# Optimization experiments

Measured on AMD Instinct MI355X. Metric: run time of the kernel, lower is better.

## Reference

```python
import jax, jax.numpy as jnp
import numpy as np

B, T, C, H = 2, 2048, 768, 12
HD = C // H  # head dim = 64
EPS = 1e-5


def layer_norm(x, g, b):
    mu = jnp.mean(x, axis=-1, keepdims=True)
    var = jnp.var(x, axis=-1, keepdims=True)
    return (x - mu) * jax.lax.rsqrt(var + EPS) * g + b


def setup_inputs() -> dict:
    key = jax.random.key(0)
    ks = jax.random.split(key, 5)
    s = 0.02
    return {
        "x": jax.random.normal(ks[0], (B, T, C), jnp.float32),
        "ln1_g": jnp.ones((C,), jnp.float32),
        "ln1_b": jnp.zeros((C,), jnp.float32),
        "W_qkv": jax.random.normal(ks[1], (C, 3 * C), jnp.float32) * s,
        "W_attn_proj": jax.random.normal(ks[2], (C, C), jnp.float32) * s,
        "ln2_g": jnp.ones((C,), jnp.float32),
        "ln2_b": jnp.zeros((C,), jnp.float32),
        "W_fc": jax.random.normal(ks[3], (C, 4 * C), jnp.float32) * s,
        "W_mlp_proj": jax.random.normal(ks[4], (4 * C, C), jnp.float32) * s,
    }


def attention(x, W_qkv, W_attn_proj):
    b, t, c = x.shape
    qkv = x @ W_qkv  # [B,T,3C]
    q, k, v = jnp.split(qkv, 3, axis=-1)
    # [B,H,T,HD]
    q = q.reshape(b, t, H, HD).transpose(0, 2, 1, 3)
    k = k.reshape(b, t, H, HD).transpose(0, 2, 1, 3)
    v = v.reshape(b, t, H, HD).transpose(0, 2, 1, 3)
    att = jnp.einsum("bhqd,bhkd->bhqk", q, k) * (1.0 / np.sqrt(HD).astype(np.float32))
    causal = jnp.tril(jnp.ones((t, t), jnp.bool_))
    att = jnp.where(causal, att, jnp.finfo(att.dtype).min)
    att = jax.nn.softmax(att, axis=-1)
    y = jnp.einsum("bhqk,bhkd->bhqd", att, v)
    y = y.transpose(0, 2, 1, 3).reshape(b, t, c)
    return y @ W_attn_proj


def mlp(x, W_fc, W_mlp_proj):
    h = jax.nn.gelu(x @ W_fc, approximate=False)
    return h @ W_mlp_proj


def reference(x, ln1_g, ln1_b, W_qkv, W_attn_proj, ln2_g, ln2_b, W_fc, W_mlp_proj):
    x = x + attention(layer_norm(x, ln1_g, ln1_b), W_qkv, W_attn_proj)
    x = x + mlp(layer_norm(x, ln2_g, ln2_b), W_fc, W_mlp_proj)
    return x
```

## Files before the change

kernel.cpp:

```cpp
#include <hip/hip_runtime.h>
#include <cstdint>
#include <cstddef>

typedef unsigned short u16;
typedef __attribute__((ext_vector_type(4))) float f32x4;
typedef __attribute__((ext_vector_type(8))) short bf16x8;

__device__ __forceinline__ u16 f2bf(float f) {
  unsigned int u = __builtin_bit_cast(unsigned int, f);
  u += 0x7fffu + ((u >> 16) & 1u);
  return (u16)(u >> 16);
}

__device__ __forceinline__ void gl_lds16(const u16* g, u16* lds_base) {
  __builtin_amdgcn_global_load_lds(
      (const __attribute__((address_space(1))) unsigned int*)g,
      (__attribute__((address_space(3))) unsigned int*)lds_base, 16, 0, 0);
}

__global__ __launch_bounds__(256) void transpose_w(const float* __restrict__ src,
                                                   u16* __restrict__ dst,
                                                   int K, int N) {
  __shared__ float tile[32][33];
  int n0 = blockIdx.x * 32, k0 = blockIdx.y * 32;
  int tx = threadIdx.x & 31, ty = threadIdx.x >> 5;
#pragma unroll
  for (int i = 0; i < 4; ++i)
    tile[ty + i * 8][tx] = src[(size_t)(k0 + ty + i * 8) * N + n0 + tx];
  __syncthreads();
#pragma unroll
  for (int i = 0; i < 4; ++i)
    dst[(size_t)(n0 + ty + i * 8) * K + k0 + tx] = f2bf(tile[tx][ty + i * 8]);
}

__global__ __launch_bounds__(256) void transpose_v(const u16* __restrict__ qkvb,
                                                   u16* __restrict__ vt) {
  __shared__ u16 tile[64 * 72];
  int t0 = blockIdx.x * 64;
  int bh = blockIdx.y;
  int b = bh / 12, h = bh % 12;
  int tid = threadIdx.x;
  int c8 = tid & 7, r = tid >> 3;
#pragma unroll
  for (int i = 0; i < 2; ++i) {
    int rr = r + i * 32;
    *(uint4*)&tile[rr * 72 + c8 * 8] =
        *(const uint4*)&qkvb[(size_t)(b * 2048 + t0 + rr) * 2304 + 1536 + h * 64 + c8 * 8];
  }
  __syncthreads();
#pragma unroll
  for (int i = 0; i < 2; ++i) {
    int dr = r + i * 32;
    u16 tmp[8];
#pragma unroll
    for (int j = 0; j < 8; ++j) tmp[j] = tile[(c8 * 8 + j) * 72 + dr];
    *(uint4*)&vt[((size_t)bh * 64 + dr) * 2048 + t0 + c8 * 8] = *(uint4*)tmp;
  }
}

__global__ void zero_counter(unsigned int* c) {
  if (threadIdx.x == 0) *c = 0u;
}

__global__ __launch_bounds__(192) void ln_rows(const float* __restrict__ x,
                                               const float* __restrict__ g,
                                               const float* __restrict__ bb,
                                               u16* __restrict__ out) {
  int row = blockIdx.x;
  int t = threadIdx.x;
  float4 v = *(const float4*)(x + (size_t)row * 768 + t * 4);
  float s = v.x + v.y + v.z + v.w;
  float sq = v.x * v.x + v.y * v.y + v.z * v.z + v.w * v.w;
#pragma unroll
  for (int o = 32; o > 0; o >>= 1) {
    s += __shfl_down(s, o);
    sq += __shfl_down(sq, o);
  }
  __shared__ float ss[3], s2[3];
  int w = t >> 6;
  if ((t & 63) == 0) { ss[w] = s; s2[w] = sq; }
  __syncthreads();
  s = ss[0] + ss[1] + ss[2];
  sq = s2[0] + s2[1] + s2[2];
  float mu = s * (1.f / 768.f);
  float var = sq * (1.f / 768.f) - mu * mu;
  float rs = rsqrtf(var + 1e-5f);
  float4 gv = *(const float4*)(g + t * 4);
  float4 bv = *(const float4*)(bb + t * 4);
  u16 o4[4];
  o4[0] = f2bf((v.x - mu) * rs * gv.x + bv.x);
  o4[1] = f2bf((v.y - mu) * rs * gv.y + bv.y);
  o4[2] = f2bf((v.z - mu) * rs * gv.z + bv.z);
  o4[3] = f2bf((v.w - mu) * rs * gv.w + bv.w);
  *(uint2*)(out + (size_t)row * 768 + t * 4) = *(uint2*)o4;
}

template <int EPI, int TN>
__global__ __launch_bounds__(256, 3) void gemm_bt(const u16* __restrict__ A,
                                                  const u16* __restrict__ BT,
                                                  int M, int N, int K,
                                                  float* __restrict__ outF,
                                                  u16* __restrict__ outB,
                                                  const float* __restrict__ res) {
  constexpr int MT = (TN == 128) ? 4 : 2;
  __shared__ __align__(16) u16 Al[128 * 64];
  __shared__ __align__(16) u16 Bl[TN * 64];
  int tid = threadIdx.x;
  int lane = tid & 63, w = tid >> 6;
  int l16 = lane & 15, quad = lane >> 4;
  int swz = l16 & 7;
  int wm = (TN == 128) ? (w >> 1) : w;
  int wn = (TN == 128) ? (w & 1) : 0;
  size_t rowA0 = (size_t)blockIdx.y * 128;
  size_t rowB0 = (size_t)blockIdx.x * TN;

  f32x4 acc[MT][4] = {};

  for (int k0 = 0; k0 < K; k0 += 64) {
    __syncthreads();
#pragma unroll
    for (int i = 0; i < 4; ++i) {
      int cbase = (i * 4 + w) * 64;
      int chunk = cbase + lane;
      int r = chunk >> 3, c8 = (chunk & 7) ^ (r & 7);
      gl_lds16(&A[(rowA0 + r) * (size_t)K + k0 + c8 * 8], &Al[cbase * 8]);
    }
#pragma unroll
    for (int i = 0; i < TN / 32; ++i) {
      int cbase = (i * 4 + w) * 64;
      int chunk = cbase + lane;
      int r = chunk >> 3, c8 = (chunk & 7) ^ (r & 7);
      gl_lds16(&BT[(rowB0 + r) * (size_t)K + k0 + c8 * 8], &Bl[cbase * 8]);
    }
    __syncthreads();
#pragma unroll
    for (int ks = 0; ks < 2; ++ks) {
      int c = ks * 4 + quad;
      bf16x8 af[MT], bf[4];
#pragma unroll
      for (int mt = 0; mt < MT; ++mt)
        af[mt] = *(const bf16x8*)&Al[(wm * (MT * 16) + mt * 16 + l16) * 64 + (c ^ swz) * 8];
#pragma unroll
      for (int nt = 0; nt < 4; ++nt)
        bf[nt] = *(const bf16x8*)&Bl[(wn * 64 + nt * 16 + l16) * 64 + (c ^ swz) * 8];
#pragma unroll
      for (int mt = 0; mt < MT; ++mt)
#pragma unroll
        for (int nt = 0; nt < 4; ++nt)
          acc[mt][nt] = __builtin_amdgcn_mfma_f32_16x16x32_bf16(af[mt], bf[nt], acc[mt][nt], 0, 0, 0);
    }
  }

#pragma unroll
  for (int mt = 0; mt < MT; ++mt) {
#pragma unroll
    for (int i = 0; i < 4; ++i) {
      size_t row = rowA0 + wm * (MT * 16) + mt * 16 + quad * 4 + i;
#pragma unroll
      for (int nt = 0; nt < 4; ++nt) {
        size_t col = rowB0 + wn * 64 + nt * 16 + l16;
        float v = acc[mt][nt][i];
        if (EPI == 0) {
          outB[row * N + col] = f2bf(v);
        } else if (EPI == 1) {
          outF[row * N + col] = res[row * N + col] + v;
        } else {
          float ge = 0.5f * v * (1.f + erff(v * 0.70710678118654752f));
          outB[row * N + col] = f2bf(ge);
        }
      }
    }
  }
}

__global__ __launch_bounds__(256, 3) void flash_attn(const u16* __restrict__ qkv,
                                                     const u16* __restrict__ vt,
                                                     u16* __restrict__ y,
                                                     unsigned int* __restrict__ ctr) {
  __shared__ __align__(16) u16 Kl[128 * 64];
  __shared__ __align__(16) u16 Vl[64 * 128];
  __shared__ __align__(16) u16 Pl[4][16 * 136];
  __shared__ unsigned int s_unit;

  int tid = threadIdx.x;
  int lane = tid & 63, w = tid >> 6;
  int l16 = lane & 15, quad = lane >> 4;
  int swz = l16 & 7;
  u16* Pw = &Pl[w][0];

  for (;;) {
    __syncthreads();
    if (tid == 0) s_unit = atomicAdd(ctr, 1u);
    __syncthreads();
    unsigned int u = s_unit;
    if (u >= 768u) return;

    int qt = 31 - (int)(u / 24u);
    int bh = (int)(u % 24u);
    int b = bh / 12, h = bh % 12;
    int qw = qt * 64 + w * 16;

    const u16* base = qkv + (size_t)b * 2048 * 2304;
    const u16* vbase = vt + (size_t)bh * 64 * 2048;

    bf16x8 qf0, qf1;
    {
      const u16* qp = base + (size_t)(qw + l16) * 2304 + h * 64 + quad * 8;
      qf0 = *(const bf16x8*)qp;
      qf1 = *(const bf16x8*)(qp + 32);
    }

    f32x4 O[4] = {};
    float l_i[4] = {0.f, 0.f, 0.f, 0.f};

    int nkb = qt / 2 + 1;
    for (int kb = 0; kb < nkb; ++kb) {
      int kt0 = kb << 7;
      __syncthreads();
#pragma unroll
      for (int i = 0; i < 4; ++i) {
        int cbase = (i * 4 + w) * 64;
        int chunk = cbase + lane;
        int r = chunk >> 3, c8 = (chunk & 7) ^ (r & 7);
        gl_lds16(base + (size_t)(kt0 + r) * 2304 + 768 + h * 64 + c8 * 8, &Kl[cbase * 8]);
      }
#pragma unroll
      for (int i = 0; i < 4; ++i) {
        int cbase = (i * 4 + w) * 64;
        int chunk = cbase + lane;
        int r = chunk >> 4, c16 = (chunk & 15) ^ (r & 7);
        gl_lds16(vbase + (size_t)r * 2048 + kt0 + c16 * 8, &Vl[cbase * 8]);
      }
      __syncthreads();

      f32x4 S[8];
#pragma unroll
      for (int nt = 0; nt < 8; ++nt) {
        bf16x8 k0 = *(const bf16x8*)&Kl[(nt * 16 + l16) * 64 + (quad ^ swz) * 8];
        bf16x8 k1 = *(const bf16x8*)&Kl[(nt * 16 + l16) * 64 + ((4 + quad) ^ swz) * 8];
        f32x4 z = {};
        z = __builtin_amdgcn_mfma_f32_16x16x32_bf16(qf0, k0, z, 0, 0, 0);
        S[nt] = __builtin_amdgcn_mfma_f32_16x16x32_bf16(qf1, k1, z, 0, 0, 0);
      }

      const float sc = 0.125f * 1.44269504088896340736f;
      bool diag = (kb == nkb - 1);
#pragma unroll
      for (int nt = 0; nt < 8; ++nt) {
        int tk = kt0 + nt * 16 + l16;
#pragma unroll
        for (int i = 0; i < 4; ++i) {
          float p = exp2f(S[nt][i] * sc);
          if (diag && tk > qw + quad * 4 + i) p = 0.f;
          l_i[i] += p;
          Pw[(quad * 4 + i) * 136 + nt * 16 + l16] =
              (u16)(__builtin_bit_cast(unsigned int, p) >> 16);
        }
      }

      asm volatile("s_waitcnt lgkmcnt(0)" ::: "memory");

#pragma unroll
      for (int c = 0; c < 4; ++c) {
        bf16x8 pf = *(const bf16x8*)&Pw[l16 * 136 + c * 32 + quad * 8];
#pragma unroll
        for (int dt = 0; dt < 4; ++dt) {
          bf16x8 vf = *(const bf16x8*)&Vl[(dt * 16 + l16) * 128 + ((c * 4 + quad) ^ swz) * 8];
          O[dt] = __builtin_amdgcn_mfma_f32_16x16x32_bf16(pf, vf, O[dt], 0, 0, 0);
        }
      }
    }

#pragma unroll
    for (int i = 0; i < 4; ++i) {
#pragma unroll
      for (int o = 1; o < 16; o <<= 1) l_i[i] += __shfl_xor(l_i[i], o);
    }
#pragma unroll
    for (int dt = 0; dt < 4; ++dt) {
#pragma unroll
      for (int i = 0; i < 4; ++i) {
        int tq = qw + quad * 4 + i;
        float ov = O[dt][i] / l_i[i];
        y[(size_t)(b * 2048 + tq) * 768 + h * 64 + dt * 16 + l16] = f2bf(ov);
      }
    }
  }
}

extern "C" void kernel_launch(void* const* d_in, const int* in_sizes, int n_in,
                              void* d_out, int out_size, void* d_ws, size_t ws_size,
                              hipStream_t stream) {
  const float* x      = (const float*)d_in[0];
  const float* ln1_g  = (const float*)d_in[1];
  const float* ln1_b  = (const float*)d_in[2];
  const float* W_qkv  = (const float*)d_in[3];
  const float* W_attn = (const float*)d_in[4];
  const float* ln2_g  = (const float*)d_in[5];
  const float* ln2_b  = (const float*)d_in[6];
  const float* W_fc   = (const float*)d_in[7];
  const float* W_mlp  = (const float*)d_in[8];
  float* out = (float*)d_out;

  const int M = 4096;
  char* p = (char*)d_ws;
  auto alloc = [&](size_t bytes) {
    char* r = p;
    p += (bytes + 255) & ~(size_t)255;
    return r;
  };
  u16* wt_qkv  = (u16*)alloc((size_t)2304 * 768 * 2);
  u16* wt_attn = (u16*)alloc((size_t)768 * 768 * 2);
  u16* wt_fc   = (u16*)alloc((size_t)3072 * 768 * 2);
  u16* wt_mlp  = (u16*)alloc((size_t)768 * 3072 * 2);
  u16* xn1     = (u16*)alloc((size_t)M * 768 * 2);
  u16* qkvb    = (u16*)alloc((size_t)M * 2304 * 2);
  u16* yb      = (u16*)alloc((size_t)M * 768 * 2);
  float* x1    = (float*)alloc((size_t)M * 768 * 4);
  u16* xn2     = (u16*)alloc((size_t)M * 768 * 2);
  u16* hb      = (u16*)alloc((size_t)M * 3072 * 2);
  u16* vt      = (u16*)alloc((size_t)24 * 64 * 2048 * 2);
  unsigned int* ctr = (unsigned int*)alloc(256);

  transpose_w<<<dim3(2304 / 32, 768 / 32), 256, 0, stream>>>(W_qkv, wt_qkv, 768, 2304);
  transpose_w<<<dim3(768 / 32, 768 / 32), 256, 0, stream>>>(W_attn, wt_attn, 768, 768);
  transpose_w<<<dim3(3072 / 32, 768 / 32), 256, 0, stream>>>(W_fc, wt_fc, 768, 3072);
  transpose_w<<<dim3(768 / 32, 3072 / 32), 256, 0, stream>>>(W_mlp, wt_mlp, 3072, 768);

  ln_rows<<<M, 192, 0, stream>>>(x, ln1_g, ln1_b, xn1);
  gemm_bt<0, 128><<<dim3(2304 / 128, M / 128), 256, 0, stream>>>(xn1, wt_qkv, M, 2304, 768,
                                                                 nullptr, qkvb, nullptr);
  transpose_v<<<dim3(32, 24), 256, 0, stream>>>(qkvb, vt);
  zero_counter<<<1, 64, 0, stream>>>(ctr);
  flash_attn<<<768, 256, 0, stream>>>(qkvb, vt, yb, ctr);
  gemm_bt<1, 64><<<dim3(768 / 64, M / 128), 256, 0, stream>>>(yb, wt_attn, M, 768, 768,
                                                              x1, nullptr, x);
  ln_rows<<<M, 192, 0, stream>>>(x1, ln2_g, ln2_b, xn2);
  gemm_bt<2, 128><<<dim3(3072 / 128, M / 128), 256, 0, stream>>>(xn2, wt_fc, M, 3072, 768,
                                                                 nullptr, hb, nullptr);
  gemm_bt<1, 64><<<dim3(768 / 64, M / 128), 256, 0, stream>>>(hb, wt_mlp, M, 768, 3072,
                                                              out, nullptr, x1);
}
```

Baseline: 283.1 us.

## Split-K the two N=768 projection GEMMs with atomic residual accumulation

The attention-projection and MLP-projection GEMMs now split K in two across blockIdx.z. Each half atomically adds its partial sums into an output buffer that a new copy kernel pre-fills with the residual. This doubles the block count on the narrow 768-wide GEMMs (192 to 384 blocks), which should fill more CUs. The cost is two extra copy launches, atomic float traffic and a nondeterministic summation order. Separately, the flash-attention softmax loop is split into a masked diagonal path and an unmasked path for off-diagonal blocks.

After: 307.3 us. 8.6% more time.

```diff
diff --git a/kernel.cpp b/kernel.cpp
--- a/kernel.cpp
+++ b/kernel.cpp
@@ -60,6 +60,12 @@
 
 __global__ void zero_counter(unsigned int* c) {
   if (threadIdx.x == 0) *c = 0u;
+}
+
+__global__ __launch_bounds__(256) void copy_f32(const float* __restrict__ src,
+                                                float* __restrict__ dst, int n4) {
+  int i = blockIdx.x * 256 + threadIdx.x;
+  if (i < n4) *(float4*)(dst + i * 4) = *(const float4*)(src + i * 4);
 }
 
 __global__ __launch_bounds__(192) void ln_rows(const float* __restrict__ x,
@@ -95,13 +101,12 @@
   *(uint2*)(out + (size_t)row * 768 + t * 4) = *(uint2*)o4;
 }
 
-template <int EPI, int TN>
+template <int EPI, int TN, int SPLITK>
 __global__ __launch_bounds__(256, 3) void gemm_bt(const u16* __restrict__ A,
                                                   const u16* __restrict__ BT,
                                                   int M, int N, int K,
                                                   float* __restrict__ outF,
-                                                  u16* __restrict__ outB,
-                                                  const float* __restrict__ res) {
+                                                  u16* __restrict__ outB) {
   constexpr int MT = (TN == 128) ? 4 : 2;
   __shared__ __align__(16) u16 Al[128 * 64];
   __shared__ __align__(16) u16 Bl[TN * 64];
@@ -113,10 +118,12 @@
   int wn = (TN == 128) ? (w & 1) : 0;
   size_t rowA0 = (size_t)blockIdx.y * 128;
   size_t rowB0 = (size_t)blockIdx.x * TN;
+  int kbeg = (SPLITK == 2) ? (int)blockIdx.z * (K >> 1) : 0;
+  int kend = (SPLITK == 2) ? kbeg + (K >> 1) : K;
 
   f32x4 acc[MT][4] = {};
 
-  for (int k0 = 0; k0 < K; k0 += 64) {
+  for (int k0 = kbeg; k0 < kend; k0 += 64) {
     __syncthreads();
 #pragma unroll
     for (int i = 0; i < 4; ++i) {
@@ -162,8 +169,8 @@
         float v = acc[mt][nt][i];
         if (EPI == 0) {
           outB[row * N + col] = f2bf(v);
-        } else if (EPI == 1) {
-          outF[row * N + col] = res[row * N + col] + v;
+        } else if (EPI == 3) {
+          atomicAdd(&outF[row * N + col], v);
         } else {
           float ge = 0.5f * v * (1.f + erff(v * 0.70710678118654752f));
           outB[row * N + col] = f2bf(ge);
@@ -214,6 +221,7 @@
     float l_i[4] = {0.f, 0.f, 0.f, 0.f};
 
     int nkb = qt / 2 + 1;
+    const float sc = 0.125f * 1.44269504088896340736f;
     for (int kb = 0; kb < nkb; ++kb) {
       int kt0 = kb << 7;
       __syncthreads();
@@ -243,19 +251,29 @@
         S[nt] = __builtin_amdgcn_mfma_f32_16x16x32_bf16(qf1, k1, z, 0, 0, 0);
       }
 
-      const float sc = 0.125f * 1.44269504088896340736f;
-      bool diag = (kb == nkb - 1);
-#pragma unroll
-      for (int nt = 0; nt < 8; ++nt) {
-        int tk = kt0 + nt * 16 + l16;
-#pragma unroll
-        for (int i = 0; i < 4; ++i) {
-          float p = exp2f(S[nt][i] * sc);
-          if (diag && tk > qw + quad * 4 + i) p = 0.f;
-          l_i[i] += p;
-          Pw[(quad * 4 + i) * 136 + nt * 16 + l16] =
-              (u16)(__builtin_bit_cast(unsigned int, p) >> 16);
+      if (kb == nkb - 1) {
+#pragma unroll
+        for (int nt = 0; nt < 8; ++nt) {
+          int tk = kt0 + nt * 16 + l16;
+#pragma unroll
+          for (int i = 0; i < 4; ++i) {
+            float p = exp2f(S[nt][i] * sc);
+            if (tk > qw + quad * 4 + i) p = 0.f;
+            l_i[i] += p;
+            Pw[(quad * 4 + i) * 136 + nt * 16 + l16] =
+                (u16)(__builtin_bit_cast(unsigned int, p) >> 16);
+          }
         }
+      } else {
+#pragma unroll
+        for (int nt = 0; nt < 8; ++nt)
+#pragma unroll
+          for (int i = 0; i < 4; ++i) {
+            float p = exp2f(S[nt][i] * sc);
+            l_i[i] += p;
+            Pw[(quad * 4 + i) * 136 + nt * 16 + l16] =
+                (u16)(__builtin_bit_cast(unsigned int, p) >> 16);
+          }
       }
 
       asm volatile("s_waitcnt lgkmcnt(0)" ::: "memory");
@@ -328,16 +346,18 @@
   transpose_w<<<dim3(768 / 32, 3072 / 32), 256, 0, stream>>>(W_mlp, wt_mlp, 3072, 768);
 
   ln_rows<<<M, 192, 0, stream>>>(x, ln1_g, ln1_b, xn1);
-  gemm_bt<0, 128><<<dim3(2304 / 128, M / 128), 256, 0, stream>>>(xn1, wt_qkv, M, 2304, 768,
-                                                                 nullptr, qkvb, nullptr);
+  gemm_bt<0, 128, 1><<<dim3(2304 / 128, M / 128), 256, 0, stream>>>(
+      xn1, wt_qkv, M, 2304, 768, nullptr, qkvb);
   transpose_v<<<dim3(32, 24), 256, 0, stream>>>(qkvb, vt);
   zero_counter<<<1, 64, 0, stream>>>(ctr);
   flash_attn<<<768, 256, 0, stream>>>(qkvb, vt, yb, ctr);
-  gemm_bt<1, 64><<<dim3(768 / 64, M / 128), 256, 0, stream>>>(yb, wt_attn, M, 768, 768,
-                                                              x1, nullptr, x);
+  copy_f32<<<(M * 768 / 4 + 255) / 256, 256, 0, stream>>>(x, x1, M * 768 / 4);
+  gemm_bt<3, 64, 2><<<dim3(768 / 64, M / 128, 2), 256, 0, stream>>>(
+      yb, wt_attn, M, 768, 768, x1, nullptr);
   ln_rows<<<M, 192, 0, stream>>>(x1, ln2_g, ln2_b, xn2);
-  gemm_bt<2, 128><<<dim3(3072 / 128, M / 128), 256, 0, stream>>>(xn2, wt_fc, M, 3072, 768,
-                                                                 nullptr, hb, nullptr);
-  gemm_bt<1, 64><<<dim3(768 / 64, M / 128), 256, 0, stream>>>(hb, wt_mlp, M, 768, 3072,
-                                                              out, nullptr, x1);
-}
+  gemm_bt<2, 128, 1><<<dim3(3072 / 128, M / 128), 256, 0, stream>>>(
+      xn2, wt_fc, M, 3072, 768, nullptr, hb);
+  copy_f32<<<(M * 768 / 4 + 255) / 256, 256, 0, stream>>>(x1, out, M * 768 / 4);
+  gemm_bt<3, 64, 2><<<dim3(768 / 64, M / 128, 2), 256, 0, stream>>>(
+      hb, wt_mlp, M, 768, 3072, out, nullptr);
+}
```

## Double-buffer GEMM LDS tiles, reshape tiles to 64-wide N, merge small launches

Applied to the files above, without the earlier changes.

The GEMM now double-buffers its LDS tiles: the next K-slice is loaded asynchronously while the current one feeds the MFMAs, which removes one barrier per iteration. Tiles become TMx64, with every wave covering TM/4 rows, so the projection GEMMs use 64x64 tiles and launch more blocks. The four weight-transpose launches are merged into one kernel, and the counter reset moves into transpose_v, which cuts kernel launches. The cost is more LDS per block, which may lower occupancy, and smaller tiles that reuse each loaded byte less.

Result: faster. 273.5 us (-3.4%).

```diff
diff --git a/kernel.cpp b/kernel.cpp
--- a/kernel.cpp
+++ b/kernel.cpp
@@ -18,11 +18,23 @@
       (__attribute__((address_space(3))) unsigned int*)lds_base, 16, 0, 0);
 }
 
-__global__ __launch_bounds__(256) void transpose_w(const float* __restrict__ src,
-                                                   u16* __restrict__ dst,
-                                                   int K, int N) {
+__global__ __launch_bounds__(256) void transpose_all(const float* __restrict__ s0,
+                                                     const float* __restrict__ s1,
+                                                     const float* __restrict__ s2,
+                                                     const float* __restrict__ s3,
+                                                     u16* __restrict__ d0,
+                                                     u16* __restrict__ d1,
+                                                     u16* __restrict__ d2,
+                                                     u16* __restrict__ d3) {
   __shared__ float tile[32][33];
-  int n0 = blockIdx.x * 32, k0 = blockIdx.y * 32;
+  int idx = blockIdx.x;
+  const float* src; u16* dst; int K, N, t;
+  if (idx < 1728)      { src = s0; dst = d0; K = 768;  N = 2304; t = idx; }
+  else if (idx < 2304) { src = s1; dst = d1; K = 768;  N = 768;  t = idx - 1728; }
+  else if (idx < 4608) { src = s2; dst = d2; K = 768;  N = 3072; t = idx - 2304; }
+  else                 { src = s3; dst = d3; K = 3072; N = 768;  t = idx - 4608; }
+  int nt_n = N >> 5;
+  int n0 = (t % nt_n) * 32, k0 = (t / nt_n) * 32;
   int tx = threadIdx.x & 31, ty = threadIdx.x >> 5;
 #pragma unroll
   for (int i = 0; i < 4; ++i)
@@ -34,8 +46,10 @@
 }
 
 __global__ __launch_bounds__(256) void transpose_v(const u16* __restrict__ qkvb,
-                                                   u16* __restrict__ vt) {
+                                                   u16* __restrict__ vt,
+                                                   unsigned int* __restrict__ ctr) {
   __shared__ u16 tile[64 * 72];
+  if (blockIdx.x == 0 && blockIdx.y == 0 && threadIdx.x == 0) *ctr = 0u;
   int t0 = blockIdx.x * 64;
   int bh = blockIdx.y;
   int b = bh / 12, h = bh % 12;
@@ -56,10 +70,6 @@
     for (int j = 0; j < 8; ++j) tmp[j] = tile[(c8 * 8 + j) * 72 + dr];
     *(uint4*)&vt[((size_t)bh * 64 + dr) * 2048 + t0 + c8 * 8] = *(uint4*)tmp;
   }
-}
-
-__global__ void zero_counter(unsigned int* c) {
-  if (threadIdx.x == 0) *c = 0u;
 }
 
 __global__ __launch_bounds__(192) void ln_rows(const float* __restrict__ x,
@@ -95,70 +105,73 @@
   *(uint2*)(out + (size_t)row * 768 + t * 4) = *(uint2*)o4;
 }
 
-template <int EPI, int TN>
+template <int EPI, int TM>
 __global__ __launch_bounds__(256, 3) void gemm_bt(const u16* __restrict__ A,
                                                   const u16* __restrict__ BT,
                                                   int M, int N, int K,
                                                   float* __restrict__ outF,
                                                   u16* __restrict__ outB,
                                                   const float* __restrict__ res) {
-  constexpr int MT = (TN == 128) ? 4 : 2;
-  __shared__ __align__(16) u16 Al[128 * 64];
-  __shared__ __align__(16) u16 Bl[TN * 64];
+  constexpr int MT = TM / 64;
+  __shared__ __align__(16) u16 Al[2][TM * 64];
+  __shared__ __align__(16) u16 Bl[2][64 * 64];
   int tid = threadIdx.x;
   int lane = tid & 63, w = tid >> 6;
   int l16 = lane & 15, quad = lane >> 4;
   int swz = l16 & 7;
-  int wm = (TN == 128) ? (w >> 1) : w;
-  int wn = (TN == 128) ? (w & 1) : 0;
-  size_t rowA0 = (size_t)blockIdx.y * 128;
-  size_t rowB0 = (size_t)blockIdx.x * TN;
-
-  f32x4 acc[MT][4] = {};
-
-  for (int k0 = 0; k0 < K; k0 += 64) {
-    __syncthreads();
-#pragma unroll
-    for (int i = 0; i < 4; ++i) {
+  size_t rowA0 = (size_t)blockIdx.y * TM;
+  size_t rowB0 = (size_t)blockIdx.x * 64;
+
+  auto stage = [&](int buf, int k0) {
+#pragma unroll
+    for (int i = 0; i < TM / 32; ++i) {
       int cbase = (i * 4 + w) * 64;
       int chunk = cbase + lane;
       int r = chunk >> 3, c8 = (chunk & 7) ^ (r & 7);
-      gl_lds16(&A[(rowA0 + r) * (size_t)K + k0 + c8 * 8], &Al[cbase * 8]);
-    }
-#pragma unroll
-    for (int i = 0; i < TN / 32; ++i) {
+      gl_lds16(&A[(rowA0 + r) * (size_t)K + k0 + c8 * 8], &Al[buf][cbase * 8]);
+    }
+#pragma unroll
+    for (int i = 0; i < 2; ++i) {
       int cbase = (i * 4 + w) * 64;
       int chunk = cbase + lane;
       int r = chunk >> 3, c8 = (chunk & 7) ^ (r & 7);
-      gl_lds16(&BT[(rowB0 + r) * (size_t)K + k0 + c8 * 8], &Bl[cbase * 8]);
-    }
+      gl_lds16(&BT[(rowB0 + r) * (size_t)K + k0 + c8 * 8], &Bl[buf][cbase * 8]);
+    }
+  };
+
+  f32x4 acc[MT][4] = {};
+  stage(0, 0);
+  int cur = 0;
+  for (int k0 = 0; k0 < K; k0 += 64) {
     __syncthreads();
+    if (k0 + 64 < K) stage(cur ^ 1, k0 + 64);
 #pragma unroll
     for (int ks = 0; ks < 2; ++ks) {
       int c = ks * 4 + quad;
       bf16x8 af[MT], bf[4];
 #pragma unroll
       for (int mt = 0; mt < MT; ++mt)
-        af[mt] = *(const bf16x8*)&Al[(wm * (MT * 16) + mt * 16 + l16) * 64 + (c ^ swz) * 8];
+        af[mt] = *(const bf16x8*)&Al[cur][(w * (TM / 4) + mt * 16 + l16) * 64 + (c ^ swz) * 8];
 #pragma unroll
       for (int nt = 0; nt < 4; ++nt)
-        bf[nt] = *(const bf16x8*)&Bl[(wn * 64 + nt * 16 + l16) * 64 + (c ^ swz) * 8];
+        bf[nt] = *(const bf16x8*)&Bl[cur][(nt * 16 + l16) * 64 + (c ^ swz) * 8];
 #pragma unroll
       for (int mt = 0; mt < MT; ++mt)
 #pragma unroll
         for (int nt = 0; nt < 4; ++nt)
           acc[mt][nt] = __builtin_amdgcn_mfma_f32_16x16x32_bf16(af[mt], bf[nt], acc[mt][nt], 0, 0, 0);
     }
+    cur ^= 1;
   }
 
 #pragma unroll
   for (int mt = 0; mt < MT; ++mt) {
 #pragma unroll
     for (int i = 0; i < 4; ++i) {
-      size_t row = rowA0 + wm * (MT * 16) + mt * 16 + quad * 4 + i;
+      size_t row = rowA0 + w * (TM / 4) + mt * 16 + quad * 4 + i;
 #pragma unroll
       for (int nt = 0; nt < 4; ++nt) {
-        size_t col = rowB0 + wn * 64 + nt * 16 + l16;
+        size_t col = rowB0 + nt * 16 + l16;
         float v = acc[mt][nt][i];
         if (EPI == 0) {
           outB[row * N + col] = f2bf(v);
@@ -214,6 +227,7 @@
     float l_i[4] = {0.f, 0.f, 0.f, 0.f};
 
     int nkb = qt / 2 + 1;
+    const float sc = 0.125f * 1.44269504088896340736f;
     for (int kb = 0; kb < nkb; ++kb) {
       int kt0 = kb << 7;
       __syncthreads();
@@ -243,7 +257,6 @@
         S[nt] = __builtin_amdgcn_mfma_f32_16x16x32_bf16(qf1, k1, z, 0, 0, 0);
       }
 
-      const float sc = 0.125f * 1.44269504088896340736f;
       bool diag = (kb == nkb - 1);
 #pragma unroll
       for (int nt = 0; nt < 8; ++nt) {
@@ -322,22 +335,19 @@
   u16* vt      = (u16*)alloc((size_t)24 * 64 * 2048 * 2);
   unsigned int* ctr = (unsigned int*)alloc(256);
 
-  transpose_w<<<dim3(2304 / 32, 768 / 32), 256, 0, stream>>>(W_qkv, wt_qkv, 768, 2304);
-  transpose_w<<<dim3(768 / 32, 768 / 32), 256, 0, stream>>>(W_attn, wt_attn, 768, 768);
-  transpose_w<<<dim3(3072 / 32, 768 / 32), 256, 0, stream>>>(W_fc, wt_fc, 768, 3072);
-  transpose_w<<<dim3(768 / 32, 3072 / 32), 256, 0, stream>>>(W_mlp, wt_mlp, 3072, 768);
+  transpose_all<<<6912, 256, 0, stream>>>(W_qkv, W_attn, W_fc, W_mlp,
+                                          wt_qkv, wt_attn, wt_fc, wt_mlp);
 
   ln_rows<<<M, 192, 0, stream>>>(x, ln1_g, ln1_b, xn1);
-  gemm_bt<0, 128><<<dim3(2304 / 128, M / 128), 256, 0, stream>>>(xn1, wt_qkv, M, 2304, 768,
-                                                                 nullptr, qkvb, nullptr);
-  transpose_v<<<dim3(32, 24), 256, 0, stream>>>(qkvb, vt);
-  zero_counter<<<1, 64, 0, stream>>>(ctr);
+  gemm_bt<0, 128><<<dim3(2304 / 64, M / 128), 256, 0, stream>>>(xn1, wt_qkv, M, 2304, 768,
+                                                                nullptr, qkvb, nullptr);
+  transpose_v<<<dim3(32, 24), 256, 0, stream>>>(qkvb, vt, ctr);
   flash_attn<<<768, 256, 0, stream>>>(qkvb, vt, yb, ctr);
-  gemm_bt<1, 64><<<dim3(768 / 64, M / 128), 256, 0, stream>>>(yb, wt_attn, M, 768, 768,
-                                                              x1, nullptr, x);
+  gemm_bt<1, 64><<<dim3(768 / 64, M / 64), 256, 0, stream>>>(yb, wt_attn, M, 768, 768,
+                                                             x1, nullptr, x);
   ln_rows<<<M, 192, 0, stream>>>(x1, ln2_g, ln2_b, xn2);
-  gemm_bt<2, 128><<<dim3(3072 / 128, M / 128), 256, 0, stream>>>(xn2, wt_fc, M, 3072, 768,
-                                                                 nullptr, hb, nullptr);
-  gemm_bt<1, 64><<<dim3(768 / 64, M / 128), 256, 0, stream>>>(hb, wt_mlp, M, 768, 3072,
-                                                              out, nullptr, x1);
-}
+  gemm_bt<2, 128><<<dim3(3072 / 64, M / 128), 256, 0, stream>>>(xn2, wt_fc, M, 3072, 768,
+                                                                nullptr, hb, nullptr);
+  gemm_bt<1, 64><<<dim3(768 / 64, M / 64), 256, 0, stream>>>(hb, wt_mlp, M, 768, 3072,
+                                                             out, nullptr, x1);
+}
```
